# Optimization experiments

Hardware: AMD Instinct MI355X
Metric: run time of the kernel (lower is better)

## Reference

```python
import jax, jax.numpy as jnp
import numpy as np

LN_EPS = 1e-5
MASK_FILL = -1e9


def setup_inputs() -> dict:
    key = jax.random.key(0)
    ks = jax.random.split(key, 10)
    B, L, D, H, O, K = 128, 2048, 128, 256, 128, 64
    return {
        "sequence_emb": jax.random.normal(ks[0], (B, L, D), jnp.float32),
        "mask": jax.random.randint(ks[1], (B, L), 0, 2, jnp.int32),
        "target_emb": jax.random.normal(ks[2], (B, D), jnp.float32),
        "pos_table": jax.random.normal(ks[3], (10000, D), jnp.float32) * 0.02,
        "W_imp1": jax.random.normal(ks[4], (3 * D, H), jnp.float32) * (1.0 / np.sqrt(3 * D)),
        "b_imp1": jnp.zeros((H,), jnp.float32),
        "W_imp2": jax.random.normal(ks[5], (H, 1), jnp.float32) * (1.0 / np.sqrt(H)),
        "b_imp2": jnp.zeros((1,), jnp.float32),
        "W_enc1": jax.random.normal(ks[6], (2 * D, H), jnp.float32) * (1.0 / np.sqrt(2 * D)),
        "b_enc1": jnp.zeros((H,), jnp.float32),
        "W_enc2": jax.random.normal(ks[7], (H, O), jnp.float32) * (1.0 / np.sqrt(H)),
        "b_enc2": jnp.zeros((O,), jnp.float32),
        "ln_gamma": jnp.ones((O,), jnp.float32),
        "ln_beta": jnp.zeros((O,), jnp.float32),
        "top_k": K,
    }


def reference(sequence_emb, mask, target_emb, pos_table, W_imp1, b_imp1, W_imp2,
              b_imp2, W_enc1, b_enc1, W_enc2, b_enc2, ln_gamma, ln_beta, top_k):
    B, L, D = sequence_emb.shape
    # position embedding lookup (positions identical across batch -> keep (L,D) and broadcast)
    positions = jnp.minimum(jnp.arange(L), pos_table.shape[0] - 1)
    pos_emb = jnp.broadcast_to(pos_table[positions][None], (B, L, D))
    combined = jnp.concatenate([sequence_emb, pos_emb], axis=-1)          # (B,L,2D)
    tgt = jnp.broadcast_to(target_emb[:, None, :], (B, L, D))
    imp_in = jnp.concatenate([combined, tgt], axis=-1)                    # (B,L,3D)
    # importance MLP -> scalar score per event
    h = jax.nn.relu(imp_in @ W_imp1 + b_imp1)
    scores = (h @ W_imp2 + b_imp2)[..., 0]                                # (B,L)
    scores = jnp.where(mask == 0, MASK_FILL, scores)
    # masked top-k, then gather in chronological (sorted-index) order
    topk_values, topk_indices = jax.lax.top_k(scores, top_k)              # (B,K)
    idx_sorted = jnp.sort(topk_indices, axis=-1)
    sel = jnp.take_along_axis(combined, idx_sorted[..., None], axis=1)    # (B,K,2D)
    encoded = jax.nn.relu(sel @ W_enc1 + b_enc1) @ W_enc2 + b_enc2        # (B,K,O)
    # reorder scores to match sorted index order (torch: gather by argsort of indices)
    order = jnp.argsort(topk_indices, axis=-1)
    topk_scores = jnp.take_along_axis(topk_values, order, axis=-1)
    attn = jax.nn.softmax(topk_scores, axis=-1)                           # (B,K)
    pooled = jnp.einsum('bk,bkd->bd', attn, encoded)                      # (B,O)
    mu = jnp.mean(pooled, axis=-1, keepdims=True)
    var = jnp.var(pooled, axis=-1, keepdims=True)
    return (pooled - mu) * jax.lax.rsqrt(var + LN_EPS) * ln_gamma + ln_beta
```

## Files before the change

### kernel.cpp

```cpp
#include <hip/hip_runtime.h>
#include <hip/hip_bf16.h>

namespace {
constexpr int NB = 128;
constexpr int NL = 2048;
constexpr int ND = 128;
constexpr int NH = 256;
constexpr int NO = 128;
constexpr int NK = 64;
constexpr int MCAP = 192;
constexpr int HTHR = 96;
constexpr int BLOOP = 8;
constexpr float MASK_FILL_F = -1e9f;
constexpr float LN_EPS_F = 1e-5f;
}

typedef __attribute__((ext_vector_type(8))) short bf16x8;
typedef __attribute__((ext_vector_type(4))) float f32x4;

__device__ __forceinline__ unsigned short bf16rne(float x) {
  unsigned u = __float_as_uint(x);
  return (unsigned short)((u + 0x7FFFu + ((u >> 16) & 1u)) >> 16);
}

__global__ __launch_bounds__(256) void k_prep(
    const float* __restrict__ W1, const float* __restrict__ pos,
    const float* __restrict__ tgt, const float* __restrict__ b1,
    const float* __restrict__ We1, const float* __restrict__ We2,
    unsigned short* __restrict__ W1aT, float* __restrict__ P,
    float* __restrict__ T, unsigned short* __restrict__ We1T,
    unsigned short* __restrict__ We2T) {
  const int blk = blockIdx.x, t = threadIdx.x;
  if (blk < ND) {
    W1aT[(size_t)t * ND + blk] = bf16rne(W1[(size_t)blk * NH + t]);
    return;
  }
  if (blk >= ND + NL + NB) {
    const int b2 = blk - (ND + NL + NB);
    if (b2 < 256) {
      We1T[(size_t)t * 256 + b2] = bf16rne(We1[(size_t)b2 * NH + t]);
    } else {
      const int d = b2 - 256;
      if (t < NO) We2T[(size_t)t * 256 + d] = bf16rne(We2[(size_t)d * NO + t]);
    }
    return;
  }
  int r, w_off, add_bias;
  const float* src;
  float* out;
  if (blk < ND + NL) {
    r = blk - ND; src = pos; out = P; w_off = ND; add_bias = 1;
  } else {
    r = blk - (ND + NL); src = tgt; out = T; w_off = 2 * ND; add_bias = 0;
  }
  __shared__ float row[ND];
  if (t < ND) row[t] = src[(size_t)r * ND + t];
  __syncthreads();
  float acc = add_bias ? b1[t] : 0.0f;
#pragma unroll 8
  for (int d = 0; d < ND; ++d)
    acc = fmaf(row[d], W1[(size_t)(w_off + d) * NH + t], acc);
  out[(size_t)r * NH + t] = acc;
}

__global__ __launch_bounds__(512, 2) void k_scores_mfma(
    const float* __restrict__ seq, const int* __restrict__ mask,
    const unsigned short* __restrict__ W1aT, const float* __restrict__ w2,
    const float* __restrict__ b2, const float* __restrict__ b1,
    const float* __restrict__ T, float* __restrict__ scores) {
  const int l0 = blockIdx.x * 128;
  const int b0 = blockIdx.y * BLOOP;
  const int t = threadIdx.x;
  const int lane = t & 63;
  const int w = t >> 6;
  const int wh = w & 3;
  const int wl = w >> 2;
  const int lh = lane & 15;
  const int kq = lane >> 4;

  __shared__ unsigned short sSeq[2][128 * 128];
  __shared__ float sRed[4][128];

  bf16x8 a[4][4];
#pragma unroll
  for (int ks = 0; ks < 4; ++ks)
#pragma unroll
    for (int mt = 0; mt < 4; ++mt)
      a[ks][mt] = *(const bf16x8*)(
          W1aT + (size_t)(wh * 64 + mt * 16 + lh) * ND + ks * 32 + kq * 8);

  float4 wv[4], b1v[4];
#pragma unroll
  for (int mt = 0; mt < 4; ++mt) {
    wv[mt] = *(const float4*)(w2 + wh * 64 + mt * 16 + kq * 4);
    b1v[mt] = *(const float4*)(b1 + wh * 64 + mt * 16 + kq * 4);
  }
  const float b2v = b2[0];

  ushort4 pf[8];
  auto prefetch = [&](int bb) {
    const float4* g = (const float4*)(seq + ((size_t)bb * NL + l0) * ND);
#pragma unroll
    for (int i = 0; i < 8; ++i) {
      const float4 f = g[t + i * 512];
      pf[i].x = bf16rne(f.x); pf[i].y = bf16rne(f.y);
      pf[i].z = bf16rne(f.z); pf[i].w = bf16rne(f.w);
    }
  };
  auto commit = [&](unsigned short* dst) {
#pragma unroll
    for (int i = 0; i < 8; ++i) {
      const int v = t + i * 512;
      const int row = v >> 5;
      const int c8 = (v & 31) * 8;
      const int off = (row << 8) + (c8 ^ ((row & 15) << 4));
      *(ushort4*)((char*)dst + off) = pf[i];
    }
  };

  prefetch(b0);
  commit((unsigned short*)sSeq[0]);
  __syncthreads();

#pragma unroll 1
  for (int j = 0; j < BLOOP; ++j) {
    const int b = b0 + j;
    unsigned short* cSeq = (unsigned short*)sSeq[j & 1];
    unsigned short* nSeq = (unsigned short*)sSeq[(j & 1) ^ 1];

    if (j + 1 < BLOOP) prefetch(b + 1);

    float4 Tv[4];
#pragma unroll
    for (int mt = 0; mt < 4; ++mt)
      Tv[mt] = *(const float4*)(T + (size_t)b * NH + wh * 64 + mt * 16 + kq * 4);

    f32x4 acc[4][4];
#pragma unroll
    for (int mt = 0; mt < 4; ++mt)
#pragma unroll
      for (int nt = 0; nt < 4; ++nt) acc[mt][nt] = (f32x4){0.f, 0.f, 0.f, 0.f};

#pragma unroll
    for (int ks = 0; ks < 4; ++ks) {
      bf16x8 Bf[4];
#pragma unroll
      for (int nt = 0; nt < 4; ++nt) {
        const int row = wl * 64 + nt * 16 + lh;
        const int off = (row << 8) + (((ks << 6) + (kq << 4)) ^ ((row & 15) << 4));
        Bf[nt] = *(const bf16x8*)((const char*)cSeq + off);
      }
#pragma unroll
      for (int mt = 0; mt < 4; ++mt)
#pragma unroll
        for (int nt = 0; nt < 4; ++nt)
          acc[mt][nt] = __builtin_amdgcn_mfma_f32_16x16x32_bf16(
              a[ks][mt], Bf[nt], acc[mt][nt], 0, 0, 0);
    }
    __syncthreads();
    if (j + 1 < BLOOP) commit(nSeq);

    float p[4] = {0.f, 0.f, 0.f, 0.f};
#pragma unroll
    for (int mt = 0; mt < 4; ++mt) {
#pragma unroll
      for (int nt = 0; nt < 4; ++nt) {
        float z;
        z = acc[mt][nt][0] + Tv[mt].x + b1v[mt].x; p[nt] = fmaf(fmaxf(z, 0.f), wv[mt].x, p[nt]);
        z = acc[mt][nt][1] + Tv[mt].y + b1v[mt].y; p[nt] = fmaf(fmaxf(z, 0.f), wv[mt].y, p[nt]);
        z = acc[mt][nt][2] + Tv[mt].z + b1v[mt].z; p[nt] = fmaf(fmaxf(z, 0.f), wv[mt].z, p[nt]);
        z = acc[mt][nt][3] + Tv[mt].w + b1v[mt].w; p[nt] = fmaf(fmaxf(z, 0.f), wv[mt].w, p[nt]);
      }
    }
#pragma unroll
    for (int nt = 0; nt < 4; ++nt) {
      float v = p[nt];
      v += __shfl_xor(v, 16);
      v += __shfl_xor(v, 32);
      if (lane < 16) sRed[wh][wl * 64 + nt * 16 + lane] = v;
    }
    __syncthreads();
    if (t < 128) {
      const int l = l0 + t;
      float sc = sRed[0][t] + sRed[1][t] + sRed[2][t] + sRed[3][t] + b2v;
      if (mask[(size_t)b * NL + l] == 0) sc = MASK_FILL_F;
      scores[(size_t)b * NL + l] = sc;
    }
  }
}

__global__ __launch_bounds__(1024, 4) void k_tail(
    const float* __restrict__ scores, const float* __restrict__ seq,
    const int* __restrict__ mask, const float* __restrict__ W1,
    const float* __restrict__ w2, const float* __restrict__ b2,
    const float* __restrict__ P, const float* __restrict__ T,
    const float* __restrict__ pos,
    const unsigned short* __restrict__ We1T, const float* __restrict__ be1,
    const unsigned short* __restrict__ We2T, const float* __restrict__ be2,
    const float* __restrict__ gamma, const float* __restrict__ beta,
    float* __restrict__ out) {
  const int b = blockIdx.x, t = threadIdx.x;
  const int lane = t & 63, w = t >> 6;
  const int lh = lane & 15, kq = lane >> 4;
  __shared__ float s_stage[128 * ND];
  unsigned* hist = (unsigned*)s_stage;
  __shared__ unsigned chunk[256];
  __shared__ unsigned suf[257];
  __shared__ int sCsel, sBsel;
  __shared__ unsigned sCntHi, sCntB, sN;
  __shared__ int s_cand[MCAP];
  __shared__ float s_cs[MCAP];
  __shared__ unsigned long long s_key[MCAP];
  __shared__ int sel_l[NK];
  __shared__ float sel_v[NK];
  __shared__ int srt_l[NK];
  __shared__ float srt_v[NK];
  __shared__ float s_at[NK];
  __shared__ unsigned short s_in[64 * 256];
  __shared__ unsigned short s_h1[64 * 256];
  __shared__ float red[4][128];
  __shared__ float rr[4];

  const unsigned mkey = ~__float_as_uint(MASK_FILL_F);
  for (int i = t; i < 4096; i += 1024) hist[i] = 0;
  if (t == 0) { sCntHi = 0; sCntB = 0; sCsel = 0; suf[256] = 0; }
  __syncthreads();
  unsigned key2[2];
#pragma unroll
  for (int i = 0; i < 2; ++i) {
    unsigned u = __float_as_uint(scores[(size_t)b * NL + t + i * 1024]);
    u = (u & 0x80000000u) ? ~u : (u | 0x80000000u);
    key2[i] = u;
    if (u != mkey) atomicAdd(&hist[u >> 20], 1u);
  }
  __syncthreads();
  if (t < 256) {
    unsigned s = 0;
#pragma unroll 4
    for (int j = 0; j < 16; ++j) s += hist[t * 16 + j];
    chunk[t] = s;
  }
  __syncthreads();
  if (t < 256) {
    unsigned s = 0;
    for (int j = t; j < 256; ++j) s += chunk[j];
    suf[t] = s;
    if (s >= (unsigned)HTHR) atomicMax(&sCsel, t);
  }
  __syncthreads();
  const int c = sCsel;
  if (t == 0) sBsel = c * 16;
  __syncthreads();
  if (t < 16) {
    unsigned s = 0;
    for (int j = c * 16 + t; j < c * 16 + 16; ++j) s += hist[j];
    if (s + suf[c + 1] >= (unsigned)HTHR) atomicMax(&sBsel, c * 16 + t);
  }
  __syncthreads();
  const unsigned B = (unsigned)sBsel;
#pragma unroll
  for (int i = 0; i < 2; ++i) {
    if (key2[i] != mkey && (key2[i] >> 20) > B) {
      unsigned pos_ = atomicAdd(&sCntHi, 1u);
      s_cand[pos_] = t + i * 1024;
    }
  }
  __syncthreads();
  const unsigned hi = sCntHi;
#pragma unroll
  for (int i = 0; i < 2; ++i) {
    if (key2[i] != mkey && (key2[i] >> 20) == B) {
      unsigned pos_ = atomicAdd(&sCntB, 1u);
      if (hi + pos_ < (unsigned)MCAP) s_cand[hi + pos_] = t + i * 1024;
    }
  }
  __syncthreads();
  if (t == 0) {
    unsigned n = sCntHi + sCntB;
    sN = (n < (unsigned)MCAP) ? n : (unsigned)MCAP;
  }
  __syncthreads();
  const int n = (int)sN;

  {
    const int hg = lane;
    const int rg = w;
    const float4* Wp = (const float4*)W1;
    const float4 wvq = ((const float4*)w2)[hg];
    const float4 Tvq = ((const float4*)(T + (size_t)b * NH))[hg];
    const float b2v = b2[0];
#pragma unroll 1
    for (int pass = 0; pass < 2; ++pass) {
      const int base = pass * 128;
      if (base >= n) break;
      const int rows_here = (n - base < 128) ? (n - base) : 128;
      __syncthreads();
#pragma unroll
      for (int i = 0; i < 4; ++i) {
        const int v = t + i * 1024;
        const int r = v >> 5, cc = v & 31;
        if (r < rows_here) {
          ((float4*)s_stage)[r * 32 + cc] =
              ((const float4*)(seq + ((size_t)b * NL + s_cand[base + r]) * ND))[cc];
        }
      }
      __syncthreads();

      if (rg * 8 < rows_here) {
        float acc[8][4];
#pragma unroll
        for (int r = 0; r < 8; ++r)
#pragma unroll
          for (int j = 0; j < 4; ++j) acc[r][j] = 0.0f;

#pragma unroll 2
        for (int d0 = 0; d0 < ND; d0 += 4) {
          float4 wq[4];
#pragma unroll
          for (int j = 0; j < 4; ++j) wq[j] = Wp[(size_t)(d0 + j) * (NH / 4) + hg];
#pragma unroll
          for (int r = 0; r < 8; ++r) {
            const float4 s = *(const float4*)&s_stage[(rg * 8 + r) * ND + d0];
            const float sv[4] = {s.x, s.y, s.z, s.w};
#pragma unroll
            for (int j = 0; j < 4; ++j) {
              acc[r][0] = fmaf(sv[j], wq[j].x, acc[r][0]);
              acc[r][1] = fmaf(sv[j], wq[j].y, acc[r][1]);
              acc[r][2] = fmaf(sv[j], wq[j].z, acc[r][2]);
              acc[r][3] = fmaf(sv[j], wq[j].w, acc[r][3]);
            }
          }
        }

#pragma unroll
        for (int r = 0; r < 8; ++r) {
          const int slot = base + rg * 8 + r;
          const int l = (slot < n) ? s_cand[slot] : 0;
          const float4 Pv = ((const float4*)(P + (size_t)l * NH))[hg];
          float z, p = 0.0f;
          z = acc[r][0] + Pv.x + Tvq.x; p = fmaf(fmaxf(z, 0.0f), wvq.x, p);
          z = acc[r][1] + Pv.y + Tvq.y; p = fmaf(fmaxf(z, 0.0f), wvq.y, p);
          z = acc[r][2] + Pv.z + Tvq.z; p = fmaf(fmaxf(z, 0.0f), wvq.z, p);
          z = acc[r][3] + Pv.w + Tvq.w; p = fmaf(fmaxf(z, 0.0f), wvq.w, p);
#pragma unroll
          for (int off = 32; off >= 1; off >>= 1) p += __shfl_xor(p, off);
          if (hg == 0 && slot < n) {
            float sc = p + b2v;
            if (mask[(size_t)b * NL + l] == 0) sc = MASK_FILL_F;
            s_cs[slot] = sc;
          }
        }
      }
    }
  }
  __syncthreads();

  for (int s = t; s < MCAP; s += 1024) {
    unsigned long long kk = 0ull;
    if (s < n) {
      unsigned u = __float_as_uint(s_cs[s]);
      u = (u & 0x80000000u) ? ~u : (u | 0x80000000u);
      const int l = s_cand[s];
      kk = ((unsigned long long)u << 11) | (unsigned long long)(NL - 1 - l);
    }
    s_key[s] = kk;
  }
  __syncthreads();
  for (int s = t; s < MCAP; s += 1024) {
    if (s < n) {
      const unsigned long long mk = s_key[s];
      int rank = 0;
      for (int j = 0; j < n; ++j) rank += (s_key[j] > mk) ? 1 : 0;
      if (rank < NK) {
        sel_l[rank] = (NL - 1) - (int)(mk & 0x7FFull);
        sel_v[rank] = s_cs[s];
      }
    }
  }
  __syncthreads();
  if (t < NK) {
    const int myl = sel_l[t];
    int pos_ = 0;
#pragma unroll 8
    for (int j = 0; j < NK; ++j) pos_ += (sel_l[j] < myl) ? 1 : 0;
    srt_l[pos_] = myl;
    srt_v[pos_] = sel_v[t];
  }
  __syncthreads();
  if (t < 64) {
    const float sc = srt_v[t];
    float m = sc;
#pragma unroll
    for (int off = 32; off >= 1; off >>= 1) m = fmaxf(m, __shfl_xor(m, off));
    const float e = expf(sc - m);
    float s = e;
#pragma unroll
    for (int off = 32; off >= 1; off >>= 1) s += __shfl_xor(s, off);
    s_at[t] = e / s;
  }
  __syncthreads();

#pragma unroll
  for (int i = 0; i < 4; ++i) {
    const int v = t + i * 1024;
    const int row = v >> 6;
    const int q = v & 63;
    const int idx = srt_l[row];
    float4 f;
    if (q < 32) f = ((const float4*)(seq + ((size_t)b * NL + idx) * ND))[q];
    else        f = ((const float4*)(pos + (size_t)idx * ND))[q - 32];
    ushort4 hv;
    hv.x = bf16rne(f.x); hv.y = bf16rne(f.y);
    hv.z = bf16rne(f.z); hv.w = bf16rne(f.w);
    const int off = (row << 9) + ((q * 8) ^ ((row & 15) << 4));
    *(ushort4*)((char*)s_in + off) = hv;
  }
  __syncthreads();

  {
    const int wh = w & 3, wn = w >> 2;
    const int row = wn * 16 + lh;
    f32x4 acc1[4];
#pragma unroll
    for (int mt = 0; mt < 4; ++mt) acc1[mt] = (f32x4){0.f, 0.f, 0.f, 0.f};
#pragma unroll
    for (int ks = 0; ks < 8; ++ks) {
      const int off = (row << 9) + ((ks * 64 + kq * 16) ^ ((row & 15) << 4));
      const bf16x8 Bf = *(const bf16x8*)((const char*)s_in + off);
#pragma unroll
      for (int mt = 0; mt < 4; ++mt) {
        const bf16x8 Af = *(const bf16x8*)(
            We1T + (size_t)(wh * 64 + mt * 16 + lh) * 256 + ks * 32 + kq * 8);
        acc1[mt] = __builtin_amdgcn_mfma_f32_16x16x32_bf16(Af, Bf, acc1[mt], 0, 0, 0);
      }
    }
#pragma unroll
    for (int mt = 0; mt < 4; ++mt) {
      const int h0 = wh * 64 + mt * 16 + kq * 4;
      const float4 bv = *(const float4*)(be1 + h0);
      const float z0 = fmaxf(acc1[mt][0] + bv.x, 0.0f);
      const float z1 = fmaxf(acc1[mt][1] + bv.y, 0.0f);
      const float z2 = fmaxf(acc1[mt][2] + bv.z, 0.0f);
      const float z3 = fmaxf(acc1[mt][3] + bv.w, 0.0f);
      const unsigned u0 = (unsigned)bf16rne(z0) | ((unsigned)bf16rne(z1) << 16);
      const unsigned u1 = (unsigned)bf16rne(z2) | ((unsigned)bf16rne(z3) << 16);
      const int off = (row << 9) + ((h0 * 2) ^ ((row & 15) << 4));
      *(unsigned*)((char*)s_h1 + off) = u0;
      *(unsigned*)((char*)s_h1 + off + 4) = u1;
    }
  }
  __syncthreads();

  if (w < 8) {
    const int wo = w & 1, wn4 = w >> 1;
    const int row = wn4 * 16 + lh;
    f32x4 acc2[4];
#pragma unroll
    for (int mt = 0; mt < 4; ++mt) acc2[mt] = (f32x4){0.f, 0.f, 0.f, 0.f};
#pragma unroll
    for (int ks = 0; ks < 8; ++ks) {
      const int off = (row << 9) + ((ks * 64 + kq * 16) ^ ((row & 15) << 4));
      const bf16x8 Bf = *(const bf16x8*)((const char*)s_h1 + off);
#pragma unroll
      for (int mt = 0; mt < 4; ++mt) {
        const bf16x8 Af = *(const bf16x8*)(
            We2T + (size_t)(wo * 64 + mt * 16 + lh) * 256 + ks * 32 + kq * 8);
        acc2[mt] = __builtin_amdgcn_mfma_f32_16x16x32_bf16(Af, Bf, acc2[mt], 0, 0, 0);
      }
    }
    const float at = s_at[row];
#pragma unroll
    for (int mt = 0; mt < 4; ++mt) {
#pragma unroll
      for (int j = 0; j < 4; ++j) {
        float v = acc2[mt][j] * at;
        v += __shfl_xor(v, 1);
        v += __shfl_xor(v, 2);
        v += __shfl_xor(v, 4);
        v += __shfl_xor(v, 8);
        if (lh == 0) red[wn4][wo * 64 + mt * 16 + kq * 4 + j] = v;
      }
    }
  }
  __syncthreads();

  float pooled = 0.0f;
  if (t < NO)
    pooled = red[0][t] + red[1][t] + red[2][t] + red[3][t] + be2[t];
  float s1 = (t < NO) ? pooled : 0.0f;
  float s2 = (t < NO) ? pooled * pooled : 0.0f;
#pragma unroll
  for (int off = 32; off >= 1; off >>= 1) {
    s1 += __shfl_xor(s1, off);
    s2 += __shfl_xor(s2, off);
  }
  if (t < NO && (t & 63) == 0) {
    rr[(t >> 6) * 2] = s1;
    rr[(t >> 6) * 2 + 1] = s2;
  }
  __syncthreads();
  if (t < NO) {
    const float S1 = rr[0] + rr[2];
    const float S2 = rr[1] + rr[3];
    const float mu = S1 / NO;
    const float var = S2 / NO - mu * mu;
    const float rs = rsqrtf(var + LN_EPS_F);
    out[(size_t)b * NO + t] = (pooled - mu) * rs * gamma[t] + beta[t];
  }
}

extern "C" void kernel_launch(void* const* d_in, const int* in_sizes, int n_in,
                              void* d_out, int out_size, void* d_ws, size_t ws_size,
                              hipStream_t stream) {
  (void)in_sizes; (void)n_in; (void)out_size; (void)ws_size;
  const float* seq = (const float*)d_in[0];
  const int* mask = (const int*)d_in[1];
  const float* tgt = (const float*)d_in[2];
  const float* pos = (const float*)d_in[3];
  const float* W1 = (const float*)d_in[4];
  const float* b1 = (const float*)d_in[5];
  const float* w2 = (const float*)d_in[6];
  const float* b2 = (const float*)d_in[7];
  const float* We1 = (const float*)d_in[8];
  const float* be1 = (const float*)d_in[9];
  const float* We2 = (const float*)d_in[10];
  const float* be2 = (const float*)d_in[11];
  const float* gam = (const float*)d_in[12];
  const float* bet = (const float*)d_in[13];
  float* out = (float*)d_out;

  float* P = (float*)d_ws;
  float* T = P + (size_t)NL * NH;
  float* scores = T + (size_t)NB * NH;
  unsigned short* w1aT = (unsigned short*)(scores + (size_t)NB * NL);
  unsigned short* we1T = w1aT + (size_t)NH * ND;
  unsigned short* we2T = we1T + (size_t)256 * 256;

  k_prep<<<ND + NL + NB + 512, 256, 0, stream>>>(W1, pos, tgt, b1, We1, We2,
                                                 w1aT, P, T, we1T, we2T);
  k_scores_mfma<<<dim3(NL / 128, NB / BLOOP), 512, 0, stream>>>(
      seq, mask, w1aT, w2, b2, b1, T, scores);
  k_tail<<<NB, 1024, 0, stream>>>(scores, seq, mask, W1, w2, b2, P, T, pos,
                                  we1T, be1, we2T, be2, gam, bet, out);
}
```

Baseline: 139.2 us.

## Split tail kernel into candidate select, parallel rescore, and encode kernels

The monolithic per-batch tail kernel is split into three launches. Histogram candidate selection runs first, then an fp32 rescoring of candidates spread over a 2D grid of 32-row tiles across batches, then selection and encoding. The encode kernel drops to 512 threads, with each wave computing two 16-row MFMA tiles. The aim is to expose more parallelism than 128 large blocks allow, at the cost of extra launches and global round-trips for candidate indices and scores.

```diff
diff --git a/kernel.cpp b/kernel.cpp
--- a/kernel.cpp
+++ b/kernel.cpp
@@ -189,11 +189,155 @@
   }
 }
 
-__global__ __launch_bounds__(1024, 4) void k_tail(
-    const float* __restrict__ scores, const float* __restrict__ seq,
-    const int* __restrict__ mask, const float* __restrict__ W1,
-    const float* __restrict__ w2, const float* __restrict__ b2,
-    const float* __restrict__ P, const float* __restrict__ T,
+__global__ __launch_bounds__(1024, 4) void k_topA(
+    const float* __restrict__ scores, int* __restrict__ cand_idx,
+    int* __restrict__ cand_n) {
+  const int b = blockIdx.x, t = threadIdx.x;
+  __shared__ unsigned hist[4096];
+  __shared__ unsigned chunk[256];
+  __shared__ unsigned suf[257];
+  __shared__ int sCsel, sBsel;
+  __shared__ unsigned sCntHi, sCntB;
+  __shared__ int s_cand[MCAP];
+
+  const unsigned mkey = ~__float_as_uint(MASK_FILL_F);
+  for (int i = t; i < 4096; i += 1024) hist[i] = 0;
+  if (t == 0) { sCntHi = 0; sCntB = 0; sCsel = 0; suf[256] = 0; }
+  __syncthreads();
+  unsigned key2[2];
+#pragma unroll
+  for (int i = 0; i < 2; ++i) {
+    unsigned u = __float_as_uint(scores[(size_t)b * NL + t + i * 1024]);
+    u = (u & 0x80000000u) ? ~u : (u | 0x80000000u);
+    key2[i] = u;
+    if (u != mkey) atomicAdd(&hist[u >> 20], 1u);
+  }
+  __syncthreads();
+  if (t < 256) {
+    unsigned s = 0;
+#pragma unroll 4
+    for (int j = 0; j < 16; ++j) s += hist[t * 16 + j];
+    chunk[t] = s;
+  }
+  __syncthreads();
+  if (t < 256) {
+    unsigned s = 0;
+    for (int j = t; j < 256; ++j) s += chunk[j];
+    suf[t] = s;
+    if (s >= (unsigned)HTHR) atomicMax(&sCsel, t);
+  }
+  __syncthreads();
+  const int c = sCsel;
+  if (t == 0) sBsel = c * 16;
+  __syncthreads();
+  if (t < 16) {
+    unsigned s = 0;
+    for (int j = c * 16 + t; j < c * 16 + 16; ++j) s += hist[j];
+    if (s + suf[c + 1] >= (unsigned)HTHR) atomicMax(&sBsel, c * 16 + t);
+  }
+  __syncthreads();
+  const unsigned B = (unsigned)sBsel;
+#pragma unroll
+  for (int i = 0; i < 2; ++i) {
+    if (key2[i] != mkey && (key2[i] >> 20) > B) {
+      unsigned pos_ = atomicAdd(&sCntHi, 1u);
+      s_cand[pos_] = t + i * 1024;
+    }
+  }
+  __syncthreads();
+  const unsigned hi = sCntHi;
+#pragma unroll
+  for (int i = 0; i < 2; ++i) {
+    if (key2[i] != mkey && (key2[i] >> 20) == B) {
+      unsigned pos_ = atomicAdd(&sCntB, 1u);
+      if (hi + pos_ < (unsigned)MCAP) s_cand[hi + pos_] = t + i * 1024;
+    }
+  }
+  __syncthreads();
+  unsigned n = sCntHi + sCntB;
+  if (n > (unsigned)MCAP) n = MCAP;
+  if (t < MCAP) cand_idx[(size_t)b * MCAP + t] = (t < (int)n) ? s_cand[t] : 0;
+  if (t == 0) cand_n[b] = (int)n;
+}
+
+__global__ __launch_bounds__(256) void k_rescoreW(
+    const float* __restrict__ seq, const int* __restrict__ mask,
+    const float* __restrict__ W1, const float* __restrict__ w2,
+    const float* __restrict__ b2, const float* __restrict__ P,
+    const float* __restrict__ T, const int* __restrict__ cand_idx,
+    const int* __restrict__ cand_n, float* __restrict__ cscore) {
+  const int b = blockIdx.y;
+  const int s0 = blockIdx.x * 32;
+  const int n = cand_n[b];
+  if (s0 >= n) return;
+  const int t = threadIdx.x;
+  __shared__ float s_seq[32 * 128];
+  __shared__ int s_l[32];
+  if (t < 32) {
+    const int slot = s0 + t;
+    s_l[t] = (slot < n) ? cand_idx[(size_t)b * MCAP + slot] : 0;
+  }
+  __syncthreads();
+#pragma unroll
+  for (int i = 0; i < 4; ++i) {
+    const int v = t + i * 256;
+    const int r = v >> 5, c = v & 31;
+    ((float4*)s_seq)[r * 32 + c] =
+        ((const float4*)(seq + ((size_t)b * NL + s_l[r]) * ND))[c];
+  }
+  __syncthreads();
+
+  const int hg = t & 63, rg = t >> 6;
+  float acc[8][4];
+#pragma unroll
+  for (int r = 0; r < 8; ++r)
+#pragma unroll
+    for (int j = 0; j < 4; ++j) acc[r][j] = 0.0f;
+
+  const float4* Wp = (const float4*)W1;
+  for (int d0 = 0; d0 < ND; d0 += 4) {
+    float4 wq[4];
+#pragma unroll
+    for (int j = 0; j < 4; ++j) wq[j] = Wp[(size_t)(d0 + j) * (NH / 4) + hg];
+#pragma unroll
+    for (int r = 0; r < 8; ++r) {
+      const float4 s = *(const float4*)&s_seq[(rg * 8 + r) * ND + d0];
+      const float sv[4] = {s.x, s.y, s.z, s.w};
+#pragma unroll
+      for (int j = 0; j < 4; ++j) {
+        acc[r][0] = fmaf(sv[j], wq[j].x, acc[r][0]);
+        acc[r][1] = fmaf(sv[j], wq[j].y, acc[r][1]);
+        acc[r][2] = fmaf(sv[j], wq[j].z, acc[r][2]);
+        acc[r][3] = fmaf(sv[j], wq[j].w, acc[r][3]);
+      }
+    }
+  }
+
+  const float4 wv = ((const float4*)w2)[hg];
+  const float4 Tv = ((const float4*)(T + (size_t)b * NH))[hg];
+  const float b2v = b2[0];
+#pragma unroll
+  for (int r = 0; r < 8; ++r) {
+    const int l = s_l[rg * 8 + r];
+    const float4 Pv = ((const float4*)(P + (size_t)l * NH))[hg];
+    float z, p = 0.0f;
+    z = acc[r][0] + Pv.x + Tv.x; p = fmaf(fmaxf(z, 0.0f), wv.x, p);
+    z = acc[r][1] + Pv.y + Tv.y; p = fmaf(fmaxf(z, 0.0f), wv.y, p);
+    z = acc[r][2] + Pv.z + Tv.z; p = fmaf(fmaxf(z, 0.0f), wv.z, p);
+    z = acc[r][3] + Pv.w + Tv.w; p = fmaf(fmaxf(z, 0.0f), wv.w, p);
+#pragma unroll
+    for (int off = 32; off >= 1; off >>= 1) p += __shfl_xor(p, off);
+    if (hg == 0) {
+      float sc = p + b2v;
+      if (mask[(size_t)b * NL + l] == 0) sc = MASK_FILL_F;
+      cscore[(size_t)b * MCAP + s0 + rg * 8 + r] = sc;
+    }
+  }
+}
+
+__global__ __launch_bounds__(512, 2) void k_selenc(
+    const float* __restrict__ cscore, const int* __restrict__ cand_idx,
+    const int* __restrict__ cand_n, const float* __restrict__ seq,
     const float* __restrict__ pos,
     const unsigned short* __restrict__ We1T, const float* __restrict__ be1,
     const unsigned short* __restrict__ We2T, const float* __restrict__ be2,
@@ -202,15 +346,8 @@
   const int b = blockIdx.x, t = threadIdx.x;
   const int lane = t & 63, w = t >> 6;
   const int lh = lane & 15, kq = lane >> 4;
-  __shared__ float s_stage[128 * ND];
-  unsigned* hist = (unsigned*)s_stage;
-  __shared__ unsigned chunk[256];
-  __shared__ unsigned suf[257];
-  __shared__ int sCsel, sBsel;
-  __shared__ unsigned sCntHi, sCntB, sN;
-  __shared__ int s_cand[MCAP];
+  __shared__ unsigned long long s_key[MCAP];
   __shared__ float s_cs[MCAP];
-  __shared__ unsigned long long s_key[MCAP];
   __shared__ int sel_l[NK];
   __shared__ float sel_v[NK];
   __shared__ int srt_l[NK];
@@ -221,152 +358,22 @@
   __shared__ float red[4][128];
   __shared__ float rr[4];
 
-  const unsigned mkey = ~__float_as_uint(MASK_FILL_F);
-  for (int i = t; i < 4096; i += 1024) hist[i] = 0;
-  if (t == 0) { sCntHi = 0; sCntB = 0; sCsel = 0; suf[256] = 0; }
-  __syncthreads();
-  unsigned key2[2];
-#pragma unroll
-  for (int i = 0; i < 2; ++i) {
-    unsigned u = __float_as_uint(scores[(size_t)b * NL + t + i * 1024]);
-    u = (u & 0x80000000u) ? ~u : (u | 0x80000000u);
-    key2[i] = u;
-    if (u != mkey) atomicAdd(&hist[u >> 20], 1u);
-  }
-  __syncthreads();
-  if (t < 256) {
-    unsigned s = 0;
-#pragma unroll 4
-    for (int j = 0; j < 16; ++j) s += hist[t * 16 + j];
-    chunk[t] = s;
-  }
-  __syncthreads();
-  if (t < 256) {
-    unsigned s = 0;
-    for (int j = t; j < 256; ++j) s += chunk[j];
-    suf[t] = s;
-    if (s >= (unsigned)HTHR) atomicMax(&sCsel, t);
-  }
-  __syncthreads();
-  const int c = sCsel;
-  if (t == 0) sBsel = c * 16;
-  __syncthreads();
-  if (t < 16) {
-    unsigned s = 0;
-    for (int j = c * 16 + t; j < c * 16 + 16; ++j) s += hist[j];
-    if (s + suf[c + 1] >= (unsigned)HTHR) atomicMax(&sBsel, c * 16 + t);
-  }
-  __syncthreads();
-  const unsigned B = (unsigned)sBsel;
-#pragma unroll
-  for (int i = 0; i < 2; ++i) {
-    if (key2[i] != mkey && (key2[i] >> 20) > B) {
-      unsigned pos_ = atomicAdd(&sCntHi, 1u);
-      s_cand[pos_] = t + i * 1024;
-    }
-  }
-  __syncthreads();
-  const unsigned hi = sCntHi;
-#pragma unroll
-  for (int i = 0; i < 2; ++i) {
-    if (key2[i] != mkey && (key2[i] >> 20) == B) {
-      unsigned pos_ = atomicAdd(&sCntB, 1u);
-      if (hi + pos_ < (unsigned)MCAP) s_cand[hi + pos_] = t + i * 1024;
-    }
-  }
-  __syncthreads();
-  if (t == 0) {
-    unsigned n = sCntHi + sCntB;
-    sN = (n < (unsigned)MCAP) ? n : (unsigned)MCAP;
-  }
-  __syncthreads();
-  const int n = (int)sN;
-
-  {
-    const int hg = lane;
-    const int rg = w;
-    const float4* Wp = (const float4*)W1;
-    const float4 wvq = ((const float4*)w2)[hg];
-    const float4 Tvq = ((const float4*)(T + (size_t)b * NH))[hg];
-    const float b2v = b2[0];
-#pragma unroll 1
-    for (int pass = 0; pass < 2; ++pass) {
-      const int base = pass * 128;
-      if (base >= n) break;
-      const int rows_here = (n - base < 128) ? (n - base) : 128;
-      __syncthreads();
-#pragma unroll
-      for (int i = 0; i < 4; ++i) {
-        const int v = t + i * 1024;
-        const int r = v >> 5, cc = v & 31;
-        if (r < rows_here) {
-          ((float4*)s_stage)[r * 32 + cc] =
-              ((const float4*)(seq + ((size_t)b * NL + s_cand[base + r]) * ND))[cc];
-        }
-      }
-      __syncthreads();
-
-      if (rg * 8 < rows_here) {
-        float acc[8][4];
-#pragma unroll
-        for (int r = 0; r < 8; ++r)
-#pragma unroll
-          for (int j = 0; j < 4; ++j) acc[r][j] = 0.0f;
-
-#pragma unroll 2
-        for (int d0 = 0; d0 < ND; d0 += 4) {
-          float4 wq[4];
-#pragma unroll
-          for (int j = 0; j < 4; ++j) wq[j] = Wp[(size_t)(d0 + j) * (NH / 4) + hg];
-#pragma unroll
-          for (int r = 0; r < 8; ++r) {
-            const float4 s = *(const float4*)&s_stage[(rg * 8 + r) * ND + d0];
-            const float sv[4] = {s.x, s.y, s.z, s.w};
-#pragma unroll
-            for (int j = 0; j < 4; ++j) {
-              acc[r][0] = fmaf(sv[j], wq[j].x, acc[r][0]);
-              acc[r][1] = fmaf(sv[j], wq[j].y, acc[r][1]);
-              acc[r][2] = fmaf(sv[j], wq[j].z, acc[r][2]);
-              acc[r][3] = fmaf(sv[j], wq[j].w, acc[r][3]);
-            }
-          }
-        }
-
-#pragma unroll
-        for (int r = 0; r < 8; ++r) {
-          const int slot = base + rg * 8 + r;
-          const int l = (slot < n) ? s_cand[slot] : 0;
-          const float4 Pv = ((const float4*)(P + (size_t)l * NH))[hg];
-          float z, p = 0.0f;
-          z = acc[r][0] + Pv.x + Tvq.x; p = fmaf(fmaxf(z, 0.0f), wvq.x, p);
-          z = acc[r][1] + Pv.y + Tvq.y; p = fmaf(fmaxf(z, 0.0f), wvq.y, p);
-          z = acc[r][2] + Pv.z + Tvq.z; p = fmaf(fmaxf(z, 0.0f), wvq.z, p);
-          z = acc[r][3] + Pv.w + Tvq.w; p = fmaf(fmaxf(z, 0.0f), wvq.w, p);
-#pragma unroll
-          for (int off = 32; off >= 1; off >>= 1) p += __shfl_xor(p, off);
-          if (hg == 0 && slot < n) {
-            float sc = p + b2v;
-            if (mask[(size_t)b * NL + l] == 0) sc = MASK_FILL_F;
-            s_cs[slot] = sc;
-          }
-        }
-      }
-    }
-  }
-  __syncthreads();
-
-  for (int s = t; s < MCAP; s += 1024) {
+  const int n = cand_n[b];
+  for (int s = t; s < MCAP; s += 512) {
     unsigned long long kk = 0ull;
+    float f = 0.0f;
     if (s < n) {
-      unsigned u = __float_as_uint(s_cs[s]);
+      f = cscore[(size_t)b * MCAP + s];
+      unsigned u = __float_as_uint(f);
       u = (u & 0x80000000u) ? ~u : (u | 0x80000000u);
-      const int l = s_cand[s];
+      const int l = cand_idx[(size_t)b * MCAP + s];
       kk = ((unsigned long long)u << 11) | (unsigned long long)(NL - 1 - l);
     }
     s_key[s] = kk;
-  }
-  __syncthreads();
-  for (int s = t; s < MCAP; s += 1024) {
+    s_cs[s] = f;
+  }
+  __syncthreads();
+  for (int s = t; s < MCAP; s += 512) {
     if (s < n) {
       const unsigned long long mk = s_key[s];
       int rank = 0;
@@ -401,8 +408,8 @@
   __syncthreads();
 
 #pragma unroll
-  for (int i = 0; i < 4; ++i) {
-    const int v = t + i * 1024;
+  for (int i = 0; i < 8; ++i) {
+    const int v = t + i * 512;
     const int row = v >> 6;
     const int q = v & 63;
     const int idx = srt_l[row];
@@ -419,39 +426,52 @@
 
   {
     const int wh = w & 3, wn = w >> 2;
-    const int row = wn * 16 + lh;
-    f32x4 acc1[4];
-#pragma unroll
-    for (int mt = 0; mt < 4; ++mt) acc1[mt] = (f32x4){0.f, 0.f, 0.f, 0.f};
+    f32x4 acc1[4][2];
+#pragma unroll
+    for (int mt = 0; mt < 4; ++mt)
+#pragma unroll
+      for (int nt = 0; nt < 2; ++nt) acc1[mt][nt] = (f32x4){0.f, 0.f, 0.f, 0.f};
 #pragma unroll
     for (int ks = 0; ks < 8; ++ks) {
-      const int off = (row << 9) + ((ks * 64 + kq * 16) ^ ((row & 15) << 4));
-      const bf16x8 Bf = *(const bf16x8*)((const char*)s_in + off);
+      bf16x8 Bf[2];
+#pragma unroll
+      for (int nt = 0; nt < 2; ++nt) {
+        const int row = wn * 32 + nt * 16 + lh;
+        const int off = (row << 9) + ((ks * 64 + kq * 16) ^ ((row & 15) << 4));
+        Bf[nt] = *(const bf16x8*)((const char*)s_in + off);
+      }
 #pragma unroll
       for (int mt = 0; mt < 4; ++mt) {
         const bf16x8 Af = *(const bf16x8*)(
             We1T + (size_t)(wh * 64 + mt * 16 + lh) * 256 + ks * 32 + kq * 8);
-        acc1[mt] = __builtin_amdgcn_mfma_f32_16x16x32_bf16(Af, Bf, acc1[mt], 0, 0, 0);
+#pragma unroll
+        for (int nt = 0; nt < 2; ++nt)
+          acc1[mt][nt] = __builtin_amdgcn_mfma_f32_16x16x32_bf16(
+              Af, Bf[nt], acc1[mt][nt], 0, 0, 0);
       }
     }
 #pragma unroll
     for (int mt = 0; mt < 4; ++mt) {
       const int h0 = wh * 64 + mt * 16 + kq * 4;
       const float4 bv = *(const float4*)(be1 + h0);
-      const float z0 = fmaxf(acc1[mt][0] + bv.x, 0.0f);
-      const float z1 = fmaxf(acc1[mt][1] + bv.y, 0.0f);
-      const float z2 = fmaxf(acc1[mt][2] + bv.z, 0.0f);
-      const float z3 = fmaxf(acc1[mt][3] + bv.w, 0.0f);
-      const unsigned u0 = (unsigned)bf16rne(z0) | ((unsigned)bf16rne(z1) << 16);
-      const unsigned u1 = (unsigned)bf16rne(z2) | ((unsigned)bf16rne(z3) << 16);
-      const int off = (row << 9) + ((h0 * 2) ^ ((row & 15) << 4));
-      *(unsigned*)((char*)s_h1 + off) = u0;
-      *(unsigned*)((char*)s_h1 + off + 4) = u1;
-    }
-  }
-  __syncthreads();
-
-  if (w < 8) {
+#pragma unroll
+      for (int nt = 0; nt < 2; ++nt) {
+        const int row = wn * 32 + nt * 16 + lh;
+        const float z0 = fmaxf(acc1[mt][nt][0] + bv.x, 0.0f);
+        const float z1 = fmaxf(acc1[mt][nt][1] + bv.y, 0.0f);
+        const float z2 = fmaxf(acc1[mt][nt][2] + bv.z, 0.0f);
+        const float z3 = fmaxf(acc1[mt][nt][3] + bv.w, 0.0f);
+        const unsigned u0 = (unsigned)bf16rne(z0) | ((unsigned)bf16rne(z1) << 16);
+        const unsigned u1 = (unsigned)bf16rne(z2) | ((unsigned)bf16rne(z3) << 16);
+        const int off = (row << 9) + ((h0 * 2) ^ ((row & 15) << 4));
+        *(unsigned*)((char*)s_h1 + off) = u0;
+        *(unsigned*)((char*)s_h1 + off + 4) = u1;
+      }
+    }
+  }
+  __syncthreads();
+
+  {
     const int wo = w & 1, wn4 = w >> 1;
     const int row = wn4 * 16 + lh;
     f32x4 acc2[4];
@@ -535,11 +555,17 @@
   unsigned short* w1aT = (unsigned short*)(scores + (size_t)NB * NL);
   unsigned short* we1T = w1aT + (size_t)NH * ND;
   unsigned short* we2T = we1T + (size_t)256 * 256;
+  int* cand_idx = (int*)(we2T + (size_t)128 * 256);
+  int* cand_n = cand_idx + (size_t)NB * MCAP;
+  float* cscore = (float*)(cand_n + NB);
 
   k_prep<<<ND + NL + NB + 512, 256, 0, stream>>>(W1, pos, tgt, b1, We1, We2,
                                                  w1aT, P, T, we1T, we2T);
   k_scores_mfma<<<dim3(NL / 128, NB / BLOOP), 512, 0, stream>>>(
       seq, mask, w1aT, w2, b2, b1, T, scores);
-  k_tail<<<NB, 1024, 0, stream>>>(scores, seq, mask, W1, w2, b2, P, T, pos,
-                                  we1T, be1, we2T, be2, gam, bet, out);
-}
+  k_topA<<<NB, 1024, 0, stream>>>(scores, cand_idx, cand_n);
+  k_rescoreW<<<dim3(MCAP / 32, NB), 256, 0, stream>>>(
+      seq, mask, W1, w2, b2, P, T, cand_idx, cand_n, cscore);
+  k_selenc<<<NB, 512, 0, stream>>>(cscore, cand_idx, cand_n, seq, pos,
+                                   we1T, be1, we2T, be2, gam, bet, out);
+}
```

Result: faster. 116.5 us (median of 2 runs) (-16.3%).
